# Optimization experiments

Measured on AMD Instinct MI355X. Metric: run time of the kernel, lower is better.

The kernel has to match this reference:

```python
import jax, jax.numpy as jnp
import numpy as np

PH, PW = 2, 2  # roi_output_h, roi_output_w


def _make_boxes(k, n):
    xy = jax.random.uniform(k, (n, 4), jnp.float32, 0.0, 7.0)
    x1 = jnp.minimum(xy[:, 0], xy[:, 2]); x2 = jnp.maximum(xy[:, 0], xy[:, 2])
    y1 = jnp.minimum(xy[:, 1], xy[:, 3]); y2 = jnp.maximum(xy[:, 1], xy[:, 3])
    return jnp.stack([x1, y1, x2, y2], axis=1)


def setup_inputs() -> dict:
    key = jax.random.key(0)
    ks = jax.random.split(key, 12)
    B, C, H, W = 8, 1280, 7, 7
    M, N = 2048, 128
    hid, ncls = 256, 20
    feature_map = jax.random.normal(ks[0], (B, C, H, W), jnp.float32)
    proposals = _make_boxes(ks[1], M)
    proposal_batch_ids = jnp.sort(jax.random.randint(ks[2], (M,), 0, B, jnp.int32))
    gt4 = _make_boxes(ks[3], N)
    labels = jax.random.randint(ks[4], (N,), 0, ncls).astype(jnp.float32)
    bboxes = jnp.concatenate([gt4, labels[:, None]], axis=1)
    bbox_batch_ids = jnp.sort(jax.random.randint(ks[5], (N,), 0, B, jnp.int32))
    W1 = 0.02 * jax.random.normal(ks[6], (C, hid), jnp.float32)
    b1 = jnp.zeros((hid,), jnp.float32)
    W2 = 0.02 * jax.random.normal(ks[7], (hid, hid), jnp.float32)
    b2 = jnp.zeros((hid,), jnp.float32)
    Wcls = 0.02 * jax.random.normal(ks[8], (hid, ncls + 1), jnp.float32)
    bcls = jnp.zeros((ncls + 1,), jnp.float32)
    Wdet = 0.02 * jax.random.normal(ks[9], (hid, 4), jnp.float32)
    bdet = jnp.zeros((4,), jnp.float32)
    return {"feature_map": feature_map, "proposals": proposals, "bboxes": bboxes,
            "W1": W1, "b1": b1, "W2": W2, "b2": b2, "Wcls": Wcls, "bcls": bcls,
            "Wdet": Wdet, "bdet": bdet,
            "proposal_batch_ids": proposal_batch_ids, "bbox_batch_ids": bbox_batch_ids}


def roi_pool(feat, rois, batch_ids, ph, pw):
    """torchvision.ops.roi_pool with spatial_scale=1.0 (quantized max pool)."""
    B, C, H, W = feat.shape
    M = rois.shape[0]
    r = jnp.round(rois)
    x1, y1, x2, y2 = r[:, 0], r[:, 1], r[:, 2], r[:, 3]
    roi_w = jnp.maximum(x2 - x1 + 1.0, 1.0)
    roi_h = jnp.maximum(y2 - y1 + 1.0, 1.0)
    bin_w = roi_w / pw
    bin_h = roi_h / ph
    rf = feat[batch_ids]                      # (M, C, H, W) irregular gather
    ys = jnp.arange(H, dtype=jnp.float32)
    xs = jnp.arange(W, dtype=jnp.float32)
    neg = jnp.float32(-jnp.inf)
    outs = []
    for i in range(ph):
        hs = jnp.clip(jnp.floor(i * bin_h) + y1, 0.0, H)
        he = jnp.clip(jnp.ceil((i + 1) * bin_h) + y1, 0.0, H)
        for j in range(pw):
            ws = jnp.clip(jnp.floor(j * bin_w) + x1, 0.0, W)
            we = jnp.clip(jnp.ceil((j + 1) * bin_w) + x1, 0.0, W)
            ymask = (ys[None, :] >= hs[:, None]) & (ys[None, :] < he[:, None])  # (M,H)
            xmask = (xs[None, :] >= ws[:, None]) & (xs[None, :] < we[:, None])  # (M,W)
            mask = ymask[:, None, :, None] & xmask[:, None, None, :]            # (M,1,H,W)
            m = jnp.where(mask, rf, neg).max(axis=(2, 3))                       # (M,C)
            empty = (he <= hs) | (we <= ws)
            outs.append(jnp.where(empty[:, None], 0.0, m))
    return jnp.stack(outs, axis=-1).reshape(M, C, ph, pw)


def pairwise_iou(p, g):
    """p: (M,4), g: (N,4) -> (M,N) IoU."""
    ix = jnp.clip(jnp.minimum(p[:, None, 2], g[None, :, 2]) - jnp.maximum(p[:, None, 0], g[None, :, 0]), 0.0)
    iy = jnp.clip(jnp.minimum(p[:, None, 3], g[None, :, 3]) - jnp.maximum(p[:, None, 1], g[None, :, 1]), 0.0)
    inter = ix * iy
    ap = (p[:, 2] - p[:, 0]) * (p[:, 3] - p[:, 1])
    ag = (g[:, 2] - g[:, 0]) * (g[:, 3] - g[:, 1])
    union = jnp.maximum(ap[:, None] + ag[None, :] - inter, 1e-6)
    return inter / union


def reference(feature_map, proposals, bboxes, W1, b1, W2, b2, Wcls, bcls, Wdet, bdet,
              proposal_batch_ids, bbox_batch_ids):
    # ROI pool + spatial mean
    roi_feat = roi_pool(feature_map, proposals, proposal_batch_ids, PH, PW)  # (M,C,2,2)
    roi_feat = roi_feat.mean(axis=(2, 3))                                    # (M,C)
    # small MLP head (dropout = identity in deterministic/eval reference)
    h = jax.nn.relu(roi_feat @ W1 + b1)
    h = h @ W2 + b2
    bbox_result = h @ Wdet + bdet   # (M,4)
    cls_result = h @ Wcls + bcls    # (M,21)
    # per-image IoU label assignment, vectorized: mask cross-image pairs
    iou = pairwise_iou(proposals, bboxes[:, :4])                              # (M,N)
    same_img = proposal_batch_ids[:, None] == bbox_batch_ids[None, :]
    iou = jnp.where(same_img, iou, 0.0)
    max_iou = iou.max(axis=1)                                                 # (M,)
    return cls_result, bbox_result, max_iou
```

## Files before the change

kernel.cpp:

```cpp
#include <hip/hip_runtime.h>
#include <math.h>

constexpr int B_ = 8, C_ = 1280, H_ = 7, W_ = 7;
constexpr int M_ = 2048, N_ = 128, HID = 256, NC = 21;
constexpr int DET_OFF = M_ * NC;
constexpr int IOU_OFF = M_ * NC + M_ * 4;
constexpr int NRECT = 784;

typedef __attribute__((ext_vector_type(8))) short bf16x8;
typedef __attribute__((ext_vector_type(8))) unsigned short u16x8;
typedef __attribute__((ext_vector_type(4))) float f32x4;

constexpr size_t W1T_OFF = 0;
constexpr size_t W2T_OFF = W1T_OFF + 655360;
constexpr size_t WHT_OFF = W2T_OFF + 131072;
constexpr size_t AM_OFF  = WHT_OFF + 16384;

constexpr int RECT_BLKS    = B_ * 40;
constexpr int PREP_W1_BLKS = 160;
constexpr int PREP_W2_BLKS = 32;
constexpr int PREP_WH_BLKS = 4;
constexpr int AUX_BLKS = RECT_BLKS + PREP_W1_BLKS + PREP_W2_BLKS + PREP_WH_BLKS;

__device__ __forceinline__ unsigned short f2bf(float f) {
    unsigned u = __builtin_bit_cast(unsigned, f);
    u += 0x7FFFu + ((u >> 16) & 1u);
    return (unsigned short)(u >> 16);
}
__device__ __forceinline__ float bf2f(unsigned short u) {
    return __builtin_bit_cast(float, (unsigned)u << 16);
}
__device__ __forceinline__ int ivix(int s, int e) {
    return s * 7 - ((s * (s - 1)) >> 1) + (e - s - 1);
}

__global__ __launch_bounds__(256) void k_aux(
    const float* __restrict__ fmap,
    const float* __restrict__ W1, const float* __restrict__ W2,
    const float* __restrict__ Wc, const float* __restrict__ Wd,
    unsigned short* __restrict__ allmax, unsigned short* __restrict__ W1t,
    unsigned short* __restrict__ W2t,    unsigned short* __restrict__ Wht)
{
    __shared__ __align__(16) float tile[32 * 49];
    __shared__ __align__(16) unsigned short rect_lds[NRECT][36];

    const int tid = threadIdx.x;
    const int b = blockIdx.x;

    if (b < RECT_BLKS) {
        int img = b / 40, c0 = (b % 40) * 32;
        const float* src = fmap + ((size_t)img * C_ + c0) * 49;
        for (int i4 = tid; i4 < 392; i4 += 256)
            *(float4*)&tile[i4 * 4] = *(const float4*)(src + i4 * 4);
        __syncthreads();

        int c = tid >> 3, sy = tid & 7;
        if (sy < 7) {
            const float* tc = tile + c * 49;
            float colacc[7];
            #pragma unroll
            for (int x = 0; x < 7; ++x) colacc[x] = -INFINITY;
            for (int ey = sy + 1; ey <= 7; ++ey) {
                int y = ey - 1;
                #pragma unroll
                for (int x = 0; x < 7; ++x)
                    colacc[x] = fmaxf(colacc[x], tc[y * 7 + x]);
                int yi = ivix(sy, ey);
                int xi = 0;
                #pragma unroll
                for (int sx = 0; sx < 7; ++sx) {
                    float mx = -INFINITY;
                    #pragma unroll
                    for (int ex = sx + 1; ex <= 7; ++ex) {
                        mx = fmaxf(mx, colacc[ex - 1]);
                        rect_lds[yi * 28 + xi][c] = f2bf(mx);
                        ++xi;
                    }
                }
            }
        }
        __syncthreads();

        unsigned short* dst = allmax + (size_t)img * NRECT * C_ + c0;
        for (int i = tid; i < NRECT * 4; i += 256) {
            int rid = i >> 2, ch = (i & 3) * 8;
            ushort4 lo = *(const ushort4*)&rect_lds[rid][ch];
            ushort4 hi = *(const ushort4*)&rect_lds[rid][ch + 4];
            unsigned short* dp = dst + (size_t)rid * C_ + ch;
            *(ushort4*)dp = lo;
            *(ushort4*)(dp + 4) = hi;
        }
    } else if (b < RECT_BLKS + PREP_W1_BLKS) {
        int k0 = (b - RECT_BLKS) * 8;
        int col = tid;
        u16x8 o;
        #pragma unroll
        for (int j = 0; j < 8; ++j) o[j] = f2bf(W1[(size_t)(k0 + j) * HID + col]);
        *(u16x8*)(W1t + (size_t)col * C_ + k0) = o;
    } else if (b < RECT_BLKS + PREP_W1_BLKS + PREP_W2_BLKS) {
        int k0 = (b - RECT_BLKS - PREP_W1_BLKS) * 8;
        int col = tid;
        u16x8 o;
        #pragma unroll
        for (int j = 0; j < 8; ++j) o[j] = f2bf(W2[(size_t)(k0 + j) * HID + col]);
        *(u16x8*)(W2t + (size_t)col * HID + k0) = o;
    } else {
        int i = (b - RECT_BLKS - PREP_W1_BLKS - PREP_W2_BLKS) * 256 + tid;
        int o32 = i & 31;
        int k0  = (i >> 5) * 8;
        u16x8 o;
        #pragma unroll
        for (int j = 0; j < 8; ++j) {
            float v = 0.0f;
            if (o32 < NC) v = Wc[(size_t)(k0 + j) * NC + o32];
            else if (o32 < NC + 4) v = Wd[(size_t)(k0 + j) * 4 + (o32 - NC)];
            o[j] = f2bf(v);
        }
        *(u16x8*)(Wht + (size_t)o32 * HID + k0) = o;
    }
}

__global__ __launch_bounds__(1024) void k_fc(
    const unsigned short* __restrict__ allmax,
    const unsigned short* __restrict__ W1t,
    const unsigned short* __restrict__ W2t,
    const unsigned short* __restrict__ Wht,
    const float* __restrict__ b1v, const float* __restrict__ b2v,
    const float* __restrict__ bc,  const float* __restrict__ bd,
    const float* __restrict__ props, const int* __restrict__ pbid,
    const float* __restrict__ bbx,   const int* __restrict__ gbid,
    float* __restrict__ out)
{
    __shared__ unsigned short featL[8][1288];
    __shared__ unsigned short h1s[16][264];
    __shared__ unsigned short h2s[16][264];
    __shared__ float gbox[N_][4];
    __shared__ int   gids[N_];

    const int tid = threadIdx.x;
    const int row0 = blockIdx.x * 8;

    if (tid < N_) {
        gbox[tid][0] = bbx[tid * 5 + 0];
        gbox[tid][1] = bbx[tid * 5 + 1];
        gbox[tid][2] = bbx[tid * 5 + 2];
        gbox[tid][3] = bbx[tid * 5 + 3];
        gids[tid] = gbid[tid];
    }

    if (tid < 512) {
        int p = tid >> 6, lane = tid & 63;
        int m = row0 + p;
        float4 bx = *(const float4*)(props + (size_t)m * 4);
        float x1 = rintf(bx.x), y1 = rintf(bx.y);
        float x2 = rintf(bx.z), y2 = rintf(bx.w);
        float rw = fmaxf(x2 - x1 + 1.0f, 1.0f);
        float rh = fmaxf(y2 - y1 + 1.0f, 1.0f);
        float bw = rw * 0.5f, bh = rh * 0.5f;
        int hs0 = __builtin_amdgcn_readfirstlane((int)fminf(fmaxf(y1, 0.f), 7.f));
        int he0 = __builtin_amdgcn_readfirstlane((int)fminf(fmaxf(ceilf(bh) + y1, 0.f), 7.f));
        int hs1 = __builtin_amdgcn_readfirstlane((int)fminf(fmaxf(floorf(bh) + y1, 0.f), 7.f));
        int he1 = __builtin_amdgcn_readfirstlane((int)fminf(fmaxf(ceilf(2.f * bh) + y1, 0.f), 7.f));
        int ws0 = __builtin_amdgcn_readfirstlane((int)fminf(fmaxf(x1, 0.f), 7.f));
        int we0 = __builtin_amdgcn_readfirstlane((int)fminf(fmaxf(ceilf(bw) + x1, 0.f), 7.f));
        int ws1 = __builtin_amdgcn_readfirstlane((int)fminf(fmaxf(floorf(bw) + x1, 0.f), 7.f));
        int we1 = __builtin_amdgcn_readfirstlane((int)fminf(fmaxf(ceilf(2.f * bw) + x1, 0.f), 7.f));
        int bid = __builtin_amdgcn_readfirstlane(pbid[m]);

        int v00 = (he0 > hs0) & (we0 > ws0);
        int v01 = (he0 > hs0) & (we1 > ws1);
        int v10 = (he1 > hs1) & (we0 > ws0);
        int v11 = (he1 > hs1) & (we1 > ws1);
        int yi0 = v00 | v01 ? ivix(hs0, max(he0, hs0 + 1)) : 0;
        int yi1 = v10 | v11 ? ivix(hs1, max(he1, hs1 + 1)) : 0;
        int xi0 = v00 | v10 ? ivix(ws0, max(we0, ws0 + 1)) : 0;
        int xi1 = v01 | v11 ? ivix(ws1, max(we1, ws1 + 1)) : 0;
        const unsigned short* base = allmax + (size_t)bid * NRECT * C_;
        const unsigned short* a00 = base + (size_t)(yi0 * 28 + xi0) * C_;
        const unsigned short* a01 = base + (size_t)(yi0 * 28 + xi1) * C_;
        const unsigned short* a10 = base + (size_t)(yi1 * 28 + xi0) * C_;
        const unsigned short* a11 = base + (size_t)(yi1 * 28 + xi1) * C_;
        float m00 = v00 ? 0.25f : 0.0f;
        float m01 = v01 ? 0.25f : 0.0f;
        float m10 = v10 ? 0.25f : 0.0f;
        float m11 = v11 ? 0.25f : 0.0f;

        #pragma unroll
        for (int it = 0; it < 5; ++it) {
            int c = it * 256 + lane * 4;
            ushort4 u0 = *(const ushort4*)(a00 + c);
            ushort4 u1 = *(const ushort4*)(a01 + c);
            ushort4 u2 = *(const ushort4*)(a10 + c);
            ushort4 u3 = *(const ushort4*)(a11 + c);
            ushort4 o;
            o.x = f2bf(bf2f(u0.x) * m00 + bf2f(u1.x) * m01 + bf2f(u2.x) * m10 + bf2f(u3.x) * m11);
            o.y = f2bf(bf2f(u0.y) * m00 + bf2f(u1.y) * m01 + bf2f(u2.y) * m10 + bf2f(u3.y) * m11);
            o.z = f2bf(bf2f(u0.z) * m00 + bf2f(u1.z) * m01 + bf2f(u2.z) * m10 + bf2f(u3.z) * m11);
            o.w = f2bf(bf2f(u0.w) * m00 + bf2f(u1.w) * m01 + bf2f(u2.w) * m10 + bf2f(u3.w) * m11);
            *(ushort4*)&featL[p][c] = o;
        }
    }
    __syncthreads();

    const int w = tid >> 6, lane = tid & 63;
    const int r = lane & 15, g = lane >> 4;
    const int col0 = w * 16;

    f32x4 acc = (f32x4){0.f, 0.f, 0.f, 0.f};
    const unsigned short* arp = featL[r & 7] + g * 8;
    const unsigned short* bp  = W1t + (size_t)(col0 + r) * C_ + g * 8;

    bf16x8 af[4], bf[4];
    #pragma unroll
    for (int i = 0; i < 4; ++i) {
        af[i] = *(const bf16x8*)(arp + i * 32);
        bf[i] = *(const bf16x8*)(bp  + i * 32);
    }
    #pragma unroll
    for (int ks = 4; ks < 40; ++ks) {
        int sl = ks & 3;
        acc = __builtin_amdgcn_mfma_f32_16x16x32_bf16(af[sl], bf[sl], acc, 0, 0, 0);
        af[sl] = *(const bf16x8*)(arp + ks * 32);
        bf[sl] = *(const bf16x8*)(bp  + ks * 32);
    }
    #pragma unroll
    for (int ks = 40; ks < 44; ++ks)
        acc = __builtin_amdgcn_mfma_f32_16x16x32_bf16(af[ks & 3], bf[ks & 3], acc, 0, 0, 0);

    {
        int col = col0 + r;
        float bias = b1v[col];
        #pragma unroll
        for (int i = 0; i < 4; ++i)
            h1s[g * 4 + i][col] = f2bf(fmaxf(acc[i] + bias, 0.f));
    }

    const unsigned short* bq = W2t + (size_t)(col0 + r) * HID + g * 8;
    bf16x8 u[8];
    #pragma unroll
    for (int ks = 0; ks < 8; ++ks) u[ks] = *(const bf16x8*)(bq + ks * 32);

    __syncthreads();

    f32x4 c2 = (f32x4){0.f, 0.f, 0.f, 0.f};
    #pragma unroll
    for (int ks = 0; ks < 8; ++ks) {
        bf16x8 a = *(const bf16x8*)(&h1s[r][ks * 32 + g * 8]);
        c2 = __builtin_amdgcn_mfma_f32_16x16x32_bf16(a, u[ks], c2, 0, 0, 0);
    }
    {
        int col = col0 + r;
        float bias = b2v[col];
        #pragma unroll
        for (int i = 0; i < 4; ++i)
            h2s[g * 4 + i][col] = f2bf(c2[i] + bias);
    }
    __syncthreads();

    if (w == 0) {
        f32x4 acc3[2];
        #pragma unroll
        for (int f = 0; f < 2; ++f) acc3[f] = (f32x4){0.f, 0.f, 0.f, 0.f};
        const unsigned short* bp3 = Wht + (size_t)r * HID + g * 8;
        #pragma unroll
        for (int ks = 0; ks < 8; ++ks) {
            bf16x8 a = *(const bf16x8*)(&h2s[r][ks * 32 + g * 8]);
            #pragma unroll
            for (int f = 0; f < 2; ++f) {
                bf16x8 b = *(const bf16x8*)(bp3 + (size_t)f * 16 * HID + ks * 32);
                acc3[f] = __builtin_amdgcn_mfma_f32_16x16x32_bf16(a, b, acc3[f], 0, 0, 0);
            }
        }
        if (g < 2) {
            #pragma unroll
            for (int f = 0; f < 2; ++f) {
                int col = f * 16 + r;
                #pragma unroll
                for (int i = 0; i < 4; ++i) {
                    int m = row0 + g * 4 + i;
                    if (col < NC)
                        out[(size_t)m * NC + col] = acc3[f][i] + bc[col];
                    else if (col < NC + 4)
                        out[DET_OFF + (size_t)m * 4 + (col - NC)] = acc3[f][i] + bd[col - NC];
                }
            }
        }
    }

    if (w < 8) {
        int m = row0 + w;
        float4 bxp = *(const float4*)(props + (size_t)m * 4);
        float ap2 = (bxp.z - bxp.x) * (bxp.w - bxp.y);
        int pb = pbid[m];
        float best = 0.0f;
        for (int n = lane; n < N_; n += 64) {
            if (gids[n] == pb) {
                float ix = fmaxf(fminf(bxp.z, gbox[n][2]) - fmaxf(bxp.x, gbox[n][0]), 0.0f);
                float iy = fmaxf(fminf(bxp.w, gbox[n][3]) - fmaxf(bxp.y, gbox[n][1]), 0.0f);
                float inter = ix * iy;
                float ag = (gbox[n][2] - gbox[n][0]) * (gbox[n][3] - gbox[n][1]);
                float un = fmaxf(ap2 + ag - inter, 1e-6f);
                best = fmaxf(best, inter / un);
            }
        }
        #pragma unroll
        for (int off = 32; off; off >>= 1)
            best = fmaxf(best, __shfl_xor(best, off));
        if (lane == 0) out[IOU_OFF + m] = best;
    }
}

extern "C" void kernel_launch(void* const* d_in, const int* in_sizes, int n_in,
                              void* d_out, int out_size, void* d_ws, size_t ws_size,
                              hipStream_t stream) {
    const float* fmap  = (const float*)d_in[0];
    const float* props = (const float*)d_in[1];
    const float* bbx   = (const float*)d_in[2];
    const float* W1    = (const float*)d_in[3];
    const float* b1v   = (const float*)d_in[4];
    const float* W2    = (const float*)d_in[5];
    const float* b2v   = (const float*)d_in[6];
    const float* Wc    = (const float*)d_in[7];
    const float* bc    = (const float*)d_in[8];
    const float* Wd    = (const float*)d_in[9];
    const float* bd    = (const float*)d_in[10];
    const int*   pbid  = (const int*)d_in[11];
    const int*   gbid  = (const int*)d_in[12];
    float* out = (float*)d_out;

    char* ws = (char*)d_ws;
    unsigned short* W1t    = (unsigned short*)(ws + W1T_OFF);
    unsigned short* W2t    = (unsigned short*)(ws + W2T_OFF);
    unsigned short* Wht    = (unsigned short*)(ws + WHT_OFF);
    unsigned short* allmax = (unsigned short*)(ws + AM_OFF);

    k_aux<<<dim3(AUX_BLKS), dim3(256), 0, stream>>>(
        fmap, W1, W2, Wc, Wd, allmax, W1t, W2t, Wht);
    k_fc<<<dim3(M_ / 8), dim3(1024), 0, stream>>>(
        allmax, W1t, W2t, Wht, b1v, b2v, bc, bd, props, pbid, bbx, gbid, out);
}
```

Measured before the change: 44.23 us.

## Merge prep and FC kernels into one cooperative kernel with grid sync

Replaces the two launches (aux prep kernel, then FC kernel) with a single cooperative kernel of 256 blocks of 1024 threads, separated by a grid-wide sync. The rectangle-max precompute is repartitioned to 64 channels per block and writes bf16 results straight to global memory instead of staging them in LDS, which gives strided 2-byte stores. The weight transpose is spread over fewer, larger blocks, and the W1 MFMA loop is restructured into a double-buffered rolling prefetch. The aim is to remove the second launch and the kernel boundary, at the cost of a grid barrier and less coalesced writes.

```diff
diff --git a/kernel.cpp b/kernel.cpp
--- a/kernel.cpp
+++ b/kernel.cpp
@@ -1,5 +1,8 @@
 #include <hip/hip_runtime.h>
+#include <hip/hip_cooperative_groups.h>
 #include <math.h>
+
+namespace cg = cooperative_groups;
 
 constexpr int B_ = 8, C_ = 1280, H_ = 7, W_ = 7;
 constexpr int M_ = 2048, N_ = 128, HID = 256, NC = 21;
@@ -16,11 +19,12 @@
 constexpr size_t WHT_OFF = W2T_OFF + 131072;
 constexpr size_t AM_OFF  = WHT_OFF + 16384;
 
-constexpr int RECT_BLKS    = B_ * 40;
-constexpr int PREP_W1_BLKS = 160;
-constexpr int PREP_W2_BLKS = 32;
-constexpr int PREP_WH_BLKS = 4;
-constexpr int AUX_BLKS = RECT_BLKS + PREP_W1_BLKS + PREP_W2_BLKS + PREP_WH_BLKS;
+struct KParams {
+    const float *fmap, *props, *bbx, *W1, *b1v, *W2, *b2v, *Wc, *bc, *Wd, *bd;
+    const int *pbid, *gbid;
+    float *out;
+    unsigned short *W1t, *W2t, *Wht, *allmax;
+};
 
 __device__ __forceinline__ unsigned short f2bf(float f) {
     unsigned u = __builtin_bit_cast(unsigned, f);
@@ -34,29 +38,39 @@
     return s * 7 - ((s * (s - 1)) >> 1) + (e - s - 1);
 }
 
-__global__ __launch_bounds__(256) void k_aux(
-    const float* __restrict__ fmap,
-    const float* __restrict__ W1, const float* __restrict__ W2,
-    const float* __restrict__ Wc, const float* __restrict__ Wd,
-    unsigned short* __restrict__ allmax, unsigned short* __restrict__ W1t,
-    unsigned short* __restrict__ W2t,    unsigned short* __restrict__ Wht)
+__global__ __launch_bounds__(1024) void k_all(KParams P)
 {
-    __shared__ __align__(16) float tile[32 * 49];
-    __shared__ __align__(16) unsigned short rect_lds[NRECT][36];
+    __shared__ __align__(16) unsigned char smem[8 * 1288 * 2];
+    __shared__ unsigned short h1s[16][264];
+    __shared__ unsigned short h2s[16][264];
+    __shared__ float gbox[N_][4];
+    __shared__ int   gids[N_];
+
+    float* tile = (float*)smem;
+    auto featL = (unsigned short (*)[1288])smem;
 
     const int tid = threadIdx.x;
-    const int b = blockIdx.x;
-
-    if (b < RECT_BLKS) {
-        int img = b / 40, c0 = (b % 40) * 32;
-        const float* src = fmap + ((size_t)img * C_ + c0) * 49;
-        for (int i4 = tid; i4 < 392; i4 += 256)
+    const int b   = blockIdx.x;
+
+    if (tid < N_) {
+        gbox[tid][0] = P.bbx[tid * 5 + 0];
+        gbox[tid][1] = P.bbx[tid * 5 + 1];
+        gbox[tid][2] = P.bbx[tid * 5 + 2];
+        gbox[tid][3] = P.bbx[tid * 5 + 3];
+        gids[tid] = P.gbid[tid];
+    }
+
+    if (b < 160) {
+        int img = b / 20, c0 = (b % 20) * 64;
+        const float* src = P.fmap + ((size_t)img * C_ + c0) * 49;
+        for (int i4 = tid; i4 < 784; i4 += 1024)
             *(float4*)&tile[i4 * 4] = *(const float4*)(src + i4 * 4);
         __syncthreads();
 
-        int c = tid >> 3, sy = tid & 7;
-        if (sy < 7) {
+        if (tid < 448) {
+            int c = tid & 63, sy = tid >> 6;
             const float* tc = tile + c * 49;
+            unsigned short* dst = P.allmax + (size_t)img * NRECT * C_ + c0 + c;
             float colacc[7];
             #pragma unroll
             for (int x = 0; x < 7; ++x) colacc[x] = -INFINITY;
@@ -73,85 +87,50 @@
                     #pragma unroll
                     for (int ex = sx + 1; ex <= 7; ++ex) {
                         mx = fmaxf(mx, colacc[ex - 1]);
-                        rect_lds[yi * 28 + xi][c] = f2bf(mx);
+                        dst[(size_t)(yi * 28 + xi) * C_] = f2bf(mx);
                         ++xi;
                     }
                 }
             }
         }
-        __syncthreads();
-
-        unsigned short* dst = allmax + (size_t)img * NRECT * C_ + c0;
-        for (int i = tid; i < NRECT * 4; i += 256) {
-            int rid = i >> 2, ch = (i & 3) * 8;
-            ushort4 lo = *(const ushort4*)&rect_lds[rid][ch];
-            ushort4 hi = *(const ushort4*)&rect_lds[rid][ch + 4];
-            unsigned short* dp = dst + (size_t)rid * C_ + ch;
-            *(ushort4*)dp = lo;
-            *(ushort4*)(dp + 4) = hi;
-        }
-    } else if (b < RECT_BLKS + PREP_W1_BLKS) {
-        int k0 = (b - RECT_BLKS) * 8;
-        int col = tid;
+    } else if (b < 200) {
+        int u = b - 160;
+        int col = tid & 255, kj = tid >> 8;
+        int k0 = u * 32 + kj * 8;
         u16x8 o;
         #pragma unroll
-        for (int j = 0; j < 8; ++j) o[j] = f2bf(W1[(size_t)(k0 + j) * HID + col]);
-        *(u16x8*)(W1t + (size_t)col * C_ + k0) = o;
-    } else if (b < RECT_BLKS + PREP_W1_BLKS + PREP_W2_BLKS) {
-        int k0 = (b - RECT_BLKS - PREP_W1_BLKS) * 8;
-        int col = tid;
+        for (int j = 0; j < 8; ++j) o[j] = f2bf(P.W1[(size_t)(k0 + j) * HID + col]);
+        *(u16x8*)(P.W1t + (size_t)col * C_ + k0) = o;
+    } else if (b < 208) {
+        int u = b - 200;
+        int col = tid & 255, kj = tid >> 8;
+        int k0 = u * 32 + kj * 8;
         u16x8 o;
         #pragma unroll
-        for (int j = 0; j < 8; ++j) o[j] = f2bf(W2[(size_t)(k0 + j) * HID + col]);
-        *(u16x8*)(W2t + (size_t)col * HID + k0) = o;
-    } else {
-        int i = (b - RECT_BLKS - PREP_W1_BLKS - PREP_W2_BLKS) * 256 + tid;
-        int o32 = i & 31;
-        int k0  = (i >> 5) * 8;
+        for (int j = 0; j < 8; ++j) o[j] = f2bf(P.W2[(size_t)(k0 + j) * HID + col]);
+        *(u16x8*)(P.W2t + (size_t)col * HID + k0) = o;
+    } else if (b == 208) {
+        int o32 = tid & 31;
+        int k0  = (tid >> 5) * 8;
         u16x8 o;
         #pragma unroll
         for (int j = 0; j < 8; ++j) {
             float v = 0.0f;
-            if (o32 < NC) v = Wc[(size_t)(k0 + j) * NC + o32];
-            else if (o32 < NC + 4) v = Wd[(size_t)(k0 + j) * 4 + (o32 - NC)];
+            if (o32 < NC) v = P.Wc[(size_t)(k0 + j) * NC + o32];
+            else if (o32 < NC + 4) v = P.Wd[(size_t)(k0 + j) * 4 + (o32 - NC)];
             o[j] = f2bf(v);
         }
-        *(u16x8*)(Wht + (size_t)o32 * HID + k0) = o;
-    }
-}
-
-__global__ __launch_bounds__(1024) void k_fc(
-    const unsigned short* __restrict__ allmax,
-    const unsigned short* __restrict__ W1t,
-    const unsigned short* __restrict__ W2t,
-    const unsigned short* __restrict__ Wht,
-    const float* __restrict__ b1v, const float* __restrict__ b2v,
-    const float* __restrict__ bc,  const float* __restrict__ bd,
-    const float* __restrict__ props, const int* __restrict__ pbid,
-    const float* __restrict__ bbx,   const int* __restrict__ gbid,
-    float* __restrict__ out)
-{
-    __shared__ unsigned short featL[8][1288];
-    __shared__ unsigned short h1s[16][264];
-    __shared__ unsigned short h2s[16][264];
-    __shared__ float gbox[N_][4];
-    __shared__ int   gids[N_];
-
-    const int tid = threadIdx.x;
-    const int row0 = blockIdx.x * 8;
-
-    if (tid < N_) {
-        gbox[tid][0] = bbx[tid * 5 + 0];
-        gbox[tid][1] = bbx[tid * 5 + 1];
-        gbox[tid][2] = bbx[tid * 5 + 2];
-        gbox[tid][3] = bbx[tid * 5 + 3];
-        gids[tid] = gbid[tid];
-    }
+        *(u16x8*)(P.Wht + (size_t)o32 * HID + k0) = o;
+    }
+
+    cg::this_grid().sync();
+
+    const int row0 = b * 8;
 
     if (tid < 512) {
         int p = tid >> 6, lane = tid & 63;
         int m = row0 + p;
-        float4 bx = *(const float4*)(props + (size_t)m * 4);
+        float4 bx = *(const float4*)(P.props + (size_t)m * 4);
         float x1 = rintf(bx.x), y1 = rintf(bx.y);
         float x2 = rintf(bx.z), y2 = rintf(bx.w);
         float rw = fmaxf(x2 - x1 + 1.0f, 1.0f);
@@ -165,7 +144,7 @@
         int we0 = __builtin_amdgcn_readfirstlane((int)fminf(fmaxf(ceilf(bw) + x1, 0.f), 7.f));
         int ws1 = __builtin_amdgcn_readfirstlane((int)fminf(fmaxf(floorf(bw) + x1, 0.f), 7.f));
         int we1 = __builtin_amdgcn_readfirstlane((int)fminf(fmaxf(ceilf(2.f * bw) + x1, 0.f), 7.f));
-        int bid = __builtin_amdgcn_readfirstlane(pbid[m]);
+        int bid = __builtin_amdgcn_readfirstlane(P.pbid[m]);
 
         int v00 = (he0 > hs0) & (we0 > ws0);
         int v01 = (he0 > hs0) & (we1 > ws1);
@@ -175,7 +154,7 @@
         int yi1 = v10 | v11 ? ivix(hs1, max(he1, hs1 + 1)) : 0;
         int xi0 = v00 | v10 ? ivix(ws0, max(we0, ws0 + 1)) : 0;
         int xi1 = v01 | v11 ? ivix(ws1, max(we1, ws1 + 1)) : 0;
-        const unsigned short* base = allmax + (size_t)bid * NRECT * C_;
+        const unsigned short* base = P.allmax + (size_t)bid * NRECT * C_;
         const unsigned short* a00 = base + (size_t)(yi0 * 28 + xi0) * C_;
         const unsigned short* a01 = base + (size_t)(yi0 * 28 + xi1) * C_;
         const unsigned short* a10 = base + (size_t)(yi1 * 28 + xi0) * C_;
@@ -208,34 +187,30 @@
 
     f32x4 acc = (f32x4){0.f, 0.f, 0.f, 0.f};
     const unsigned short* arp = featL[r & 7] + g * 8;
-    const unsigned short* bp  = W1t + (size_t)(col0 + r) * C_ + g * 8;
-
-    bf16x8 af[4], bf[4];
-    #pragma unroll
-    for (int i = 0; i < 4; ++i) {
-        af[i] = *(const bf16x8*)(arp + i * 32);
-        bf[i] = *(const bf16x8*)(bp  + i * 32);
-    }
-    #pragma unroll
-    for (int ks = 4; ks < 40; ++ks) {
-        int sl = ks & 3;
-        acc = __builtin_amdgcn_mfma_f32_16x16x32_bf16(af[sl], bf[sl], acc, 0, 0, 0);
-        af[sl] = *(const bf16x8*)(arp + ks * 32);
-        bf[sl] = *(const bf16x8*)(bp  + ks * 32);
-    }
-    #pragma unroll
-    for (int ks = 40; ks < 44; ++ks)
-        acc = __builtin_amdgcn_mfma_f32_16x16x32_bf16(af[ks & 3], bf[ks & 3], acc, 0, 0, 0);
+    const unsigned short* bp  = P.W1t + (size_t)(col0 + r) * C_ + g * 8;
+
+    bf16x8 aA = *(const bf16x8*)arp;
+    bf16x8 bA = *(const bf16x8*)bp;
+    bf16x8 aB = *(const bf16x8*)(arp + 32);
+    bf16x8 bB = *(const bf16x8*)(bp + 32);
+    for (int ks = 2; ks < 40; ++ks) {
+        bf16x8 aN = *(const bf16x8*)(arp + ks * 32);
+        bf16x8 bN = *(const bf16x8*)(bp  + ks * 32);
+        acc = __builtin_amdgcn_mfma_f32_16x16x32_bf16(aA, bA, acc, 0, 0, 0);
+        aA = aB; bA = bB; aB = aN; bB = bN;
+    }
+    acc = __builtin_amdgcn_mfma_f32_16x16x32_bf16(aA, bA, acc, 0, 0, 0);
+    acc = __builtin_amdgcn_mfma_f32_16x16x32_bf16(aB, bB, acc, 0, 0, 0);
 
     {
         int col = col0 + r;
-        float bias = b1v[col];
+        float bias = P.b1v[col];
         #pragma unroll
         for (int i = 0; i < 4; ++i)
             h1s[g * 4 + i][col] = f2bf(fmaxf(acc[i] + bias, 0.f));
     }
 
-    const unsigned short* bq = W2t + (size_t)(col0 + r) * HID + g * 8;
+    const unsigned short* bq = P.W2t + (size_t)(col0 + r) * HID + g * 8;
     bf16x8 u[8];
     #pragma unroll
     for (int ks = 0; ks < 8; ++ks) u[ks] = *(const bf16x8*)(bq + ks * 32);
@@ -250,7 +225,7 @@
     }
     {
         int col = col0 + r;
-        float bias = b2v[col];
+        float bias = P.b2v[col];
         #pragma unroll
         for (int i = 0; i < 4; ++i)
             h2s[g * 4 + i][col] = f2bf(c2[i] + bias);
@@ -261,14 +236,14 @@
         f32x4 acc3[2];
         #pragma unroll
         for (int f = 0; f < 2; ++f) acc3[f] = (f32x4){0.f, 0.f, 0.f, 0.f};
-        const unsigned short* bp3 = Wht + (size_t)r * HID + g * 8;
+        const unsigned short* bp3 = P.Wht + (size_t)r * HID + g * 8;
         #pragma unroll
         for (int ks = 0; ks < 8; ++ks) {
             bf16x8 a = *(const bf16x8*)(&h2s[r][ks * 32 + g * 8]);
             #pragma unroll
             for (int f = 0; f < 2; ++f) {
-                bf16x8 b = *(const bf16x8*)(bp3 + (size_t)f * 16 * HID + ks * 32);
-                acc3[f] = __builtin_amdgcn_mfma_f32_16x16x32_bf16(a, b, acc3[f], 0, 0, 0);
+                bf16x8 bb = *(const bf16x8*)(bp3 + (size_t)f * 16 * HID + ks * 32);
+                acc3[f] = __builtin_amdgcn_mfma_f32_16x16x32_bf16(a, bb, acc3[f], 0, 0, 0);
             }
         }
         if (g < 2) {
@@ -279,9 +254,9 @@
                 for (int i = 0; i < 4; ++i) {
                     int m = row0 + g * 4 + i;
                     if (col < NC)
-                        out[(size_t)m * NC + col] = acc3[f][i] + bc[col];
+                        P.out[(size_t)m * NC + col] = acc3[f][i] + P.bc[col];
                     else if (col < NC + 4)
-                        out[DET_OFF + (size_t)m * 4 + (col - NC)] = acc3[f][i] + bd[col - NC];
+                        P.out[DET_OFF + (size_t)m * 4 + (col - NC)] = acc3[f][i] + P.bd[col - NC];
                 }
             }
         }
@@ -289,9 +264,9 @@
 
     if (w < 8) {
         int m = row0 + w;
-        float4 bxp = *(const float4*)(props + (size_t)m * 4);
+        float4 bxp = *(const float4*)(P.props + (size_t)m * 4);
         float ap2 = (bxp.z - bxp.x) * (bxp.w - bxp.y);
-        int pb = pbid[m];
+        int pb = P.pbid[m];
         float best = 0.0f;
         for (int n = lane; n < N_; n += 64) {
             if (gids[n] == pb) {
@@ -306,36 +281,34 @@
         #pragma unroll
         for (int off = 32; off; off >>= 1)
             best = fmaxf(best, __shfl_xor(best, off));
-        if (lane == 0) out[IOU_OFF + m] = best;
+        if (lane == 0) P.out[IOU_OFF + m] = best;
     }
 }
 
 extern "C" void kernel_launch(void* const* d_in, const int* in_sizes, int n_in,
                               void* d_out, int out_size, void* d_ws, size_t ws_size,
                               hipStream_t stream) {
-    const float* fmap  = (const float*)d_in[0];
-    const float* props = (const float*)d_in[1];
-    const float* bbx   = (const float*)d_in[2];
-    const float* W1    = (const float*)d_in[3];
-    const float* b1v   = (const float*)d_in[4];
-    const float* W2    = (const float*)d_in[5];
-    const float* b2v   = (const float*)d_in[6];
-    const float* Wc    = (const float*)d_in[7];
-    const float* bc    = (const float*)d_in[8];
-    const float* Wd    = (const float*)d_in[9];
-    const float* bd    = (const float*)d_in[10];
-    const int*   pbid  = (const int*)d_in[11];
-    const int*   gbid  = (const int*)d_in[12];
-    float* out = (float*)d_out;
-
     char* ws = (char*)d_ws;
-    unsigned short* W1t    = (unsigned short*)(ws + W1T_OFF);
-    unsigned short* W2t    = (unsigned short*)(ws + W2T_OFF);
-    unsigned short* Wht    = (unsigned short*)(ws + WHT_OFF);
-    unsigned short* allmax = (unsigned short*)(ws + AM_OFF);
-
-    k_aux<<<dim3(AUX_BLKS), dim3(256), 0, stream>>>(
-        fmap, W1, W2, Wc, Wd, allmax, W1t, W2t, Wht);
-    k_fc<<<dim3(M_ / 8), dim3(1024), 0, stream>>>(
-        allmax, W1t, W2t, Wht, b1v, b2v, bc, bd, props, pbid, bbx, gbid, out);
-}
+    KParams prm;
+    prm.fmap   = (const float*)d_in[0];
+    prm.props  = (const float*)d_in[1];
+    prm.bbx    = (const float*)d_in[2];
+    prm.W1     = (const float*)d_in[3];
+    prm.b1v    = (const float*)d_in[4];
+    prm.W2     = (const float*)d_in[5];
+    prm.b2v    = (const float*)d_in[6];
+    prm.Wc     = (const float*)d_in[7];
+    prm.bc     = (const float*)d_in[8];
+    prm.Wd     = (const float*)d_in[9];
+    prm.bd     = (const float*)d_in[10];
+    prm.pbid   = (const int*)d_in[11];
+    prm.gbid   = (const int*)d_in[12];
+    prm.out    = (float*)d_out;
+    prm.W1t    = (unsigned short*)(ws + W1T_OFF);
+    prm.W2t    = (unsigned short*)(ws + W2T_OFF);
+    prm.Wht    = (unsigned short*)(ws + WHT_OFF);
+    prm.allmax = (unsigned short*)(ws + AM_OFF);
+
+    void* args[] = {&prm};
+    hipLaunchCooperativeKernel((void*)k_all, dim3(256), dim3(1024), args, 0, stream);
+}
```

Result: slower. 88.70 us (+100.5%).
